# Kernel optimization log

Measured on AMD Instinct MI355X. Metric: run time of the kernel, lower is better.

The kernel has to match this reference:

```python
import jax, jax.numpy as jnp
import numpy as np

N_NODES = 100000


def _gcn_conv(x, W, b, src, dst, n):
    # PyG GCNConv: add self-loops, sym-normalize by deg^{-1/2}, then X W + b
    h = x @ W  # [N, out]
    ones = jnp.ones(src.shape[0], dtype=x.dtype)
    deg = jax.ops.segment_sum(ones, dst, num_segments=n) + 1.0  # +1 for self loop
    dinv = jax.lax.rsqrt(deg)
    norm = dinv[src] * dinv[dst]  # [E]
    agg = jax.ops.segment_sum(h[src] * norm[:, None], dst, num_segments=n)
    agg = agg + h * (dinv * dinv)[:, None]  # self-loop contribution
    return agg + b


def setup_inputs() -> dict:
    key = jax.random.key(0)
    k1, k2, k3, k4 = jax.random.split(key, 4)
    n, e = N_NODES, 1600000
    in_d, hid_d, out_d = 128, 128, 64
    x = jax.random.normal(k1, (n, in_d), dtype=jnp.float32)
    edge_index = jax.random.randint(k2, (2, e), 0, n, dtype=jnp.int64)
    s1 = 1.0 / np.sqrt(in_d)
    s2 = 1.0 / np.sqrt(hid_d)
    W1 = jax.random.uniform(k3, (in_d, hid_d), jnp.float32, -s1, s1)
    W2 = jax.random.uniform(k4, (hid_d, out_d), jnp.float32, -s2, s2)
    b1 = jnp.zeros((hid_d,), jnp.float32)
    b2 = jnp.zeros((out_d,), jnp.float32)
    return {"x": x, "edge_index": edge_index, "W1": W1, "b1": b1, "W2": W2, "b2": b2}


def reference(x, edge_index, W1, b1, W2, b2):
    src, dst = edge_index[0], edge_index[1]
    n = x.shape[0]
    h = _gcn_conv(x, W1, b1, src, dst, n)
    h = jax.nn.relu(h)
    # dropout p=0.2 is identity at eval time
    out = _gcn_conv(h, W2, b2, src, dst, n)
    return out
```

## Files before the change

### kernel.cpp

```cpp
#include <hip/hip_runtime.h>


typedef unsigned int u32;
using bfrag = __attribute__((ext_vector_type(8))) short;
using f4    = __attribute__((ext_vector_type(4))) float;

__device__ inline u32 pack_bf16(float a, float b) {
    u32 ua = __float_as_uint(a);
    u32 ub = __float_as_uint(b);
    ua += 0x7fffu + ((ua >> 16) & 1u);
    ub += 0x7fffu + ((ub >> 16) & 1u);
    return (ua >> 16) | (ub & 0xffff0000u);
}
__device__ inline float bf_lo(u32 v) { return __uint_as_float(v << 16); }
__device__ inline float bf_hi(u32 v) { return __uint_as_float(v & 0xffff0000u); }

__device__ inline u32 pack_w(float w) {
    u32 b = __float_as_uint(w) + 0x800u;
    if (b < 0x3B800000u) b = 0x3B800000u;
    if (b > 0x3F800000u) b = 0x3F800000u;
    return (b - 0x3B800000u) >> 12;
}
__device__ inline float dec_w(u32 e) {
    return __uint_as_float(((e & 0x7fffu) << 12) + 0x3B800000u);
}

__device__ inline bfrag as_bfrag(uint4 v) {
    union { uint4 u; bfrag b; } x; x.u = v; return x.b;
}


__global__ __launch_bounds__(256) void count_bins(const int* __restrict__ dst,
                                                  int* __restrict__ bc,
                                                  int E, int nbin, int nb3) {
    __shared__ int hist[512];
    for (int t = threadIdx.x; t < nbin; t += 256) hist[t] = 0;
    __syncthreads();
    const int base = blockIdx.x * 2048 + threadIdx.x;
#pragma unroll
    for (int k = 0; k < 8; ++k) {
        int e = base + k * 256;
        if (e < E) atomicAdd(&hist[dst[e] >> 8], 1);
    }
    __syncthreads();
    for (int t = threadIdx.x; t < nbin; t += 256)
        bc[(size_t)t * nb3 + blockIdx.x] = hist[t];
}

__global__ __launch_bounds__(1024) void scan_reduce_g(const int* __restrict__ a,
                                                      int* __restrict__ bsum, int M) {
    __shared__ int wsum[16];
    int i = blockIdx.x * 1024 + threadIdx.x;
    int v = (i < M) ? a[i] : 0;
#pragma unroll
    for (int off = 32; off > 0; off >>= 1) v += __shfl_down(v, off);
    const int lane = threadIdx.x & 63;
    const int wid  = threadIdx.x >> 6;
    if (lane == 0) wsum[wid] = v;
    __syncthreads();
    if (threadIdx.x < 16) {
        int s = wsum[threadIdx.x];
#pragma unroll
        for (int off = 8; off > 0; off >>= 1) s += __shfl_down(s, off);
        if (threadIdx.x == 0) bsum[blockIdx.x] = s;
    }
}

__global__ void scan_partials(const int* __restrict__ bsum, int* __restrict__ boff,
                              int* __restrict__ total_out, int nb) {
    const int lane = threadIdx.x;
    int carry = 0;
    for (int base = 0; base < nb; base += 64) {
        int i = base + lane;
        int v = (i < nb) ? bsum[i] : 0;
        int x = v;
#pragma unroll
        for (int off = 1; off < 64; off <<= 1) {
            int t = __shfl_up(x, off);
            if (lane >= off) x += t;
        }
        if (i < nb) boff[i] = carry + x - v;
        carry += __shfl(x, 63);
    }
    if (lane == 0) *total_out = carry;
}

__global__ __launch_bounds__(1024) void scan_apply_g(int* __restrict__ a,
                                                     const int* __restrict__ boff, int M) {
    __shared__ int wsum[16];
    const int lane = threadIdx.x & 63;
    const int wid  = threadIdx.x >> 6;
    int i = blockIdx.x * 1024 + threadIdx.x;
    int v = (i < M) ? a[i] : 0;
    int x = v;
#pragma unroll
    for (int off = 1; off < 64; off <<= 1) {
        int t = __shfl_up(x, off);
        if (lane >= off) x += t;
    }
    if (lane == 63) wsum[wid] = x;
    __syncthreads();
    if (wid == 0 && lane < 16) {
        int w = wsum[lane];
#pragma unroll
        for (int off = 1; off < 16; off <<= 1) {
            int t = __shfl_up(w, off);
            if (lane >= off) w += t;
        }
        wsum[lane] = w;
    }
    __syncthreads();
    int wave_excl = (wid == 0) ? 0 : wsum[wid - 1];
    if (i < M) a[i] = boff[blockIdx.x] + wave_excl + (x - v);
}

__global__ __launch_bounds__(1024) void scan_apply_cnt(const int* __restrict__ cnt,
                                                       const int* __restrict__ boff,
                                                       int* __restrict__ row_ptr,
                                                       float* __restrict__ dinv, int n) {
    __shared__ int wsum[16];
    const int lane = threadIdx.x & 63;
    const int wid  = threadIdx.x >> 6;
    int i = blockIdx.x * 1024 + threadIdx.x;
    int v = (i < n) ? cnt[i] : 0;
    int x = v;
#pragma unroll
    for (int off = 1; off < 64; off <<= 1) {
        int t = __shfl_up(x, off);
        if (lane >= off) x += t;
    }
    if (lane == 63) wsum[wid] = x;
    __syncthreads();
    if (wid == 0 && lane < 16) {
        int w = wsum[lane];
#pragma unroll
        for (int off = 1; off < 16; off <<= 1) {
            int t = __shfl_up(w, off);
            if (lane >= off) w += t;
        }
        wsum[lane] = w;
    }
    __syncthreads();
    int wave_excl = (wid == 0) ? 0 : wsum[wid - 1];
    if (i < n) {
        row_ptr[i] = boff[blockIdx.x] + wave_excl + (x - v);
        dinv[i]    = rsqrtf((float)v + 1.0f);
    }
}

__global__ __launch_bounds__(256) void scatter_bins(const int* __restrict__ src,
                                                    const int* __restrict__ dst,
                                                    const int* __restrict__ offs,
                                                    u32* __restrict__ tmp,
                                                    int E, int nbin, int nb3) {
    __shared__ int cur[512];
    for (int t = threadIdx.x; t < nbin; t += 256)
        cur[t] = offs[(size_t)t * nb3 + blockIdx.x];
    __syncthreads();
    const int base = blockIdx.x * 2048 + threadIdx.x;
#pragma unroll
    for (int k = 0; k < 8; ++k) {
        int e = base + k * 256;
        if (e < E) {
            int d = dst[e];
            int pos = atomicAdd(&cur[d >> 8], 1);
            tmp[pos] = ((u32)(d & 255) << 17) | (u32)src[e];
        }
    }
}

__global__ __launch_bounds__(256) void bucket_csr(const u32* __restrict__ tmp,
                                                  const int* __restrict__ offs,
                                                  u32* __restrict__ tmp3,
                                                  int* __restrict__ cnt,
                                                  int n, int nb3) {
    __shared__ int hist[256];
    __shared__ int cur[256];
    __shared__ int wtot[4];
    const int b   = blockIdx.x;
    const int beg = offs[(size_t)b * nb3];
    const int end = offs[(size_t)(b + 1) * nb3];
    hist[threadIdx.x] = 0;
    __syncthreads();
    for (int i = beg + threadIdx.x; i < end; i += 256)
        atomicAdd(&hist[tmp[i] >> 17], 1);
    __syncthreads();
    const int lane = threadIdx.x & 63;
    const int wid  = threadIdx.x >> 6;
    int v = hist[threadIdx.x];
    int x = v;
#pragma unroll
    for (int off = 1; off < 64; off <<= 1) {
        int t = __shfl_up(x, off);
        if (lane >= off) x += t;
    }
    if (lane == 63) wtot[wid] = x;
    __syncthreads();
    int wbase = 0;
    for (int w = 0; w < wid; ++w) wbase += wtot[w];
    cur[threadIdx.x] = beg + wbase + x - v;
    int d = b * 256 + threadIdx.x;
    if (d < n) cnt[d] = v;
    __syncthreads();
    for (int i = beg + threadIdx.x; i < end; i += 256) {
        u32 r = tmp[i];
        int pos = atomicAdd(&cur[r >> 17], 1);
        tmp3[pos] = r & 0x1ffffu;
    }
}

__global__ __launch_bounds__(256) void build_ew(const u32* __restrict__ tmp3,
                                                const int* __restrict__ row_ptr,
                                                const float* __restrict__ dinv,
                                                u32* __restrict__ ew, int n) {
    int d = blockIdx.x * 256 + threadIdx.x;
    if (d >= n) return;
    float dd = dinv[d];
    int beg = row_ptr[d], end = row_ptr[d + 1];
    for (int i = beg; i < end; ++i) {
        u32 s = tmp3[i];
        ew[i] = (s << 15) | pack_w(dinv[s] * dd);
    }
}


__global__ void prep_w(const float* __restrict__ W1, const float* __restrict__ W2,
                       u32* __restrict__ W1t, u32* __restrict__ W2t) {
    int idx = blockIdx.x * 256 + threadIdx.x;
    if (idx < 128 * 64) {
        int nr = idx >> 6, kd = idx & 63;
        W1t[idx] = pack_bf16(W1[(2 * kd) * 128 + nr], W1[(2 * kd + 1) * 128 + nr]);
    } else if (idx < 128 * 64 + 64 * 64) {
        int i = idx - 128 * 64;
        int nr = i >> 6, kd = i & 63;
        W2t[i] = pack_bf16(W2[(2 * kd) * 64 + nr], W2[(2 * kd + 1) * 64 + nr]);
    }
}

template <int OUT, bool ABF>
__global__ __launch_bounds__(256) void gemm_mfma(const void* __restrict__ Ap,
                                                 const u32* __restrict__ Wt,
                                                 u32* __restrict__ C, int n) {
    constexpr int NT = OUT / 16;
    const int lane = threadIdx.x & 63;
    const int wv   = threadIdx.x >> 6;
    const int r15  = lane & 15;
    const int quad = lane >> 4;
    const int rowbase = blockIdx.x * 128 + wv * 32;

    bfrag af[2][4];
#pragma unroll
    for (int mi = 0; mi < 2; ++mi) {
        int row = rowbase + mi * 16 + r15;
        row = (row < n) ? row : (n - 1);
        if constexpr (ABF) {
            const u32* ar = (const u32*)Ap + (size_t)row * 64 + quad * 4;
#pragma unroll
            for (int ks = 0; ks < 4; ++ks)
                af[mi][ks] = as_bfrag(*(const uint4*)(ar + ks * 16));
        } else {
            const float* arf = (const float*)Ap + (size_t)row * 128 + quad * 8;
#pragma unroll
            for (int ks = 0; ks < 4; ++ks) {
                float4 v0 = *(const float4*)(arf + ks * 32);
                float4 v1 = *(const float4*)(arf + ks * 32 + 4);
                uint4 p;
                p.x = pack_bf16(v0.x, v0.y);
                p.y = pack_bf16(v0.z, v0.w);
                p.z = pack_bf16(v1.x, v1.y);
                p.w = pack_bf16(v1.z, v1.w);
                af[mi][ks] = as_bfrag(p);
            }
        }
    }

    f4 acc[2][NT];
#pragma unroll
    for (int mi = 0; mi < 2; ++mi)
#pragma unroll
        for (int nt = 0; nt < NT; ++nt) acc[mi][nt] = (f4)0.0f;

#pragma unroll
    for (int nt = 0; nt < NT; ++nt) {
        const u32* wr = Wt + (size_t)(nt * 16 + r15) * 64 + quad * 4;
#pragma unroll
        for (int ks = 0; ks < 4; ++ks) {
            bfrag bf = as_bfrag(*(const uint4*)(wr + ks * 16));
            acc[0][nt] = __builtin_amdgcn_mfma_f32_16x16x32_bf16(bf, af[0][ks], acc[0][nt], 0, 0, 0);
            acc[1][nt] = __builtin_amdgcn_mfma_f32_16x16x32_bf16(bf, af[1][ks], acc[1][nt], 0, 0, 0);
        }
    }

#pragma unroll
    for (int mi = 0; mi < 2; ++mi) {
        int row = rowbase + mi * 16 + r15;
        if (row < n) {
            u32* cp = C + (size_t)row * (OUT / 2);
#pragma unroll
            for (int nt = 0; nt < NT; ++nt) {
                uint2 p;
                p.x = pack_bf16(acc[mi][nt][0], acc[mi][nt][1]);
                p.y = pack_bf16(acc[mi][nt][2], acc[mi][nt][3]);
                *(uint2*)(cp + nt * 8 + quad * 2) = p;
            }
        }
    }
}


__global__ __launch_bounds__(256) void gather128(const u32* __restrict__ h,
                                                 const float* __restrict__ dinv,
                                                 const int* __restrict__ row_ptr,
                                                 const u32* __restrict__ ew,
                                                 const float* __restrict__ bias,
                                                 u32* __restrict__ outp, int n) {
    const int lane = threadIdx.x & 63;
    int node = blockIdx.x * 4 + (threadIdx.x >> 6);
    if (node >= n) return;
    node = __builtin_amdgcn_readfirstlane(node);

    const float dd  = dinv[node];
    const int   beg = __builtin_amdgcn_readfirstlane(row_ptr[node]);
    const int   end = __builtin_amdgcn_readfirstlane(row_ptr[node + 1]);

    u32 sv = h[(size_t)node * 64 + lane];
    float2 b = ((const float2*)bias)[lane];
    float acc0 = fmaf(bf_lo(sv) * dd, dd, b.x);
    float acc1 = fmaf(bf_hi(sv) * dd, dd, b.y);

    int j = beg;
    for (; j + 16 <= end; j += 16) {
        u32 ep[16];
#pragma unroll
        for (int k = 0; k < 16; ++k) ep[k] = ew[j + k];
        u32 v[16];
#pragma unroll
        for (int k = 0; k < 16; ++k)
            v[k] = h[((size_t)(ep[k] >> 15) << 6) + lane];
#pragma unroll
        for (int k = 0; k < 16; ++k) {
            float wf = dec_w(ep[k]);
            acc0 = fmaf(wf, bf_lo(v[k]), acc0);
            acc1 = fmaf(wf, bf_hi(v[k]), acc1);
        }
    }
    for (; j < end; j += 8) {
        const int cnt = end - j;
        u32 ep[8];
#pragma unroll
        for (int k = 0; k < 8; ++k) {
            int c = j + k;
            ep[k] = ew[(c < end) ? c : end - 1];
        }
        u32 v[8];
#pragma unroll
        for (int k = 0; k < 8; ++k)
            v[k] = h[((size_t)(ep[k] >> 15) << 6) + lane];
#pragma unroll
        for (int k = 0; k < 8; ++k) {
            float wf = (k < cnt) ? dec_w(ep[k]) : 0.0f;
            acc0 = fmaf(wf, bf_lo(v[k]), acc0);
            acc1 = fmaf(wf, bf_hi(v[k]), acc1);
        }
    }

    outp[(size_t)node * 64 + lane] = pack_bf16(fmaxf(acc0, 0.0f), fmaxf(acc1, 0.0f));
}

__global__ __launch_bounds__(256) void gather64(const u32* __restrict__ h,
                                                const float* __restrict__ dinv,
                                                const int* __restrict__ row_ptr,
                                                const u32* __restrict__ ew,
                                                const float* __restrict__ bias,
                                                float* __restrict__ outp, int n) {
    const int lane   = threadIdx.x & 63;
    const int lane32 = lane & 31;
    const int sub    = lane >> 5;
    int node = blockIdx.x * 4 + (threadIdx.x >> 6);
    if (node >= n) return;
    node = __builtin_amdgcn_readfirstlane(node);

    const int beg = __builtin_amdgcn_readfirstlane(row_ptr[node]);
    const int end = __builtin_amdgcn_readfirstlane(row_ptr[node + 1]);

    float acc0 = 0.0f, acc1 = 0.0f;
    if (sub == 0) {
        const float dd = dinv[node];
        u32 sv = h[(size_t)node * 32 + lane32];
        float2 b = ((const float2*)bias)[lane32];
        acc0 = fmaf(bf_lo(sv) * dd, dd, b.x);
        acc1 = fmaf(bf_hi(sv) * dd, dd, b.y);
    }

    int j = beg;
    for (; j + 8 <= end; j += 8) {
        u32 ep[8];
#pragma unroll
        for (int k = 0; k < 8; ++k) ep[k] = ew[j + k];
        u32 v[4]; float wl[4];
#pragma unroll
        for (int p = 0; p < 4; ++p) {
            u32 e0 = ep[2 * p], e1 = ep[2 * p + 1];
            u32 so = sub ? (e1 >> 15) : (e0 >> 15);
            wl[p]  = sub ? dec_w(e1) : dec_w(e0);
            v[p]   = h[((size_t)so << 5) + lane32];
        }
#pragma unroll
        for (int p = 0; p < 4; ++p) {
            acc0 = fmaf(wl[p], bf_lo(v[p]), acc0);
            acc1 = fmaf(wl[p], bf_hi(v[p]), acc1);
        }
    }
    for (; j < end; j += 8) {
        const int cnt = end - j;
        u32 ep[8];
#pragma unroll
        for (int k = 0; k < 8; ++k) {
            int c = j + k;
            ep[k] = ew[(c < end) ? c : end - 1];
        }
        u32 v[4]; float wl[4];
#pragma unroll
        for (int p = 0; p < 4; ++p) {
            u32 e0 = ep[2 * p], e1 = ep[2 * p + 1];
            float w0 = (2 * p     < cnt) ? dec_w(e0) : 0.0f;
            float w1 = (2 * p + 1 < cnt) ? dec_w(e1) : 0.0f;
            u32 so = sub ? (e1 >> 15) : (e0 >> 15);
            wl[p]  = sub ? w1 : w0;
            v[p]   = h[((size_t)so << 5) + lane32];
        }
#pragma unroll
        for (int p = 0; p < 4; ++p) {
            acc0 = fmaf(wl[p], bf_lo(v[p]), acc0);
            acc1 = fmaf(wl[p], bf_hi(v[p]), acc1);
        }
    }

    acc0 += __shfl_xor(acc0, 32);
    acc1 += __shfl_xor(acc1, 32);
    if (sub == 0)
        ((float2*)(outp + (size_t)node * 64))[lane32] = make_float2(acc0, acc1);
}

extern "C" void kernel_launch(void* const* d_in, const int* in_sizes, int n_in,
                              void* d_out, int out_size, void* d_ws, size_t ws_size,
                              hipStream_t stream) {
    const float* x  = (const float*)d_in[0];
    const int*   ei = (const int*)d_in[1];
    const float* W1 = (const float*)d_in[2];
    const float* b1 = (const float*)d_in[3];
    const float* W2 = (const float*)d_in[4];
    const float* b2 = (const float*)d_in[5];
    float*       out = (float*)d_out;

    const int n = in_sizes[0] / 128;
    const int E = in_sizes[1] / 2;
    const int* srcv = ei;
    const int* dstv = ei + E;

    const int NP = 102400;
    u32* wsd = (u32*)d_ws;
    float* dinv    = (float*)wsd;
    int*   row_ptr = (int*)(wsd + NP);
    u32*   ew      = wsd + 2 * (size_t)NP;
    u32*   h1u     = ew + E;
    u32*   agg1b   = h1u + (size_t)n * 64;
    u32*   W1t     = agg1b + (size_t)n * 64;
    u32*   W2t     = W1t + 8192;
    u32*   h2u     = h1u;

    int*   cnt  = (int*)h1u;
    int*   bco  = (int*)(h1u + 131072);
    u32*   tmp2 = h1u + 524288;
    u32*   tmp3 = tmp2 + (size_t)E;
    int*   bsum = (int*)(h1u + 4000000);
    int*   boff = bsum + 512;

    const int NBIN = (n + 255) >> 8;
    const int NB3  = (E + 2047) / 2048;
    const int M    = NBIN * NB3;
    const int MB   = (M + 1023) / 1024;
    const int NB   = (n + 1023) / 1024;

    count_bins<<<NB3, 256, 0, stream>>>(dstv, bco, E, NBIN, NB3);
    scan_reduce_g<<<MB, 1024, 0, stream>>>(bco, bsum, M);
    scan_partials<<<1, 64, 0, stream>>>(bsum, boff, bco + M, MB);
    scan_apply_g<<<MB, 1024, 0, stream>>>(bco, boff, M);
    scatter_bins<<<NB3, 256, 0, stream>>>(srcv, dstv, bco, tmp2, E, NBIN, NB3);
    bucket_csr<<<NBIN, 256, 0, stream>>>(tmp2, bco, tmp3, cnt, n, NB3);
    scan_reduce_g<<<NB, 1024, 0, stream>>>(cnt, bsum, n);
    scan_partials<<<1, 64, 0, stream>>>(bsum, boff, row_ptr + n, NB);
    scan_apply_cnt<<<NB, 1024, 0, stream>>>(cnt, boff, row_ptr, dinv, n);
    build_ew<<<(n + 255) / 256, 256, 0, stream>>>(tmp3, row_ptr, dinv, ew, n);

    prep_w<<<48, 256, 0, stream>>>(W1, W2, W1t, W2t);

    const int gblocks = (n + 127) / 128;
    gemm_mfma<128, false><<<gblocks, 256, 0, stream>>>(x, W1t, h1u, n);
    gather128<<<(n + 3) / 4, 256, 0, stream>>>(h1u, dinv, row_ptr, ew, b1, agg1b, n);

    gemm_mfma<64, true><<<gblocks, 256, 0, stream>>>(agg1b, W2t, h2u, n);
    gather64<<<(n + 3) / 4, 256, 0, stream>>>(h2u, dinv, row_ptr, ew, b2, out, n);
}
```

Baseline: 313.2 us.

## Slice feature matrices into 16-column slabs for cache-local gathers

The GEMMs now write their bf16 outputs in a slab layout: each 16-feature slice of all nodes is stored contiguously (32 bytes per node). The gathers are rewritten so each block handles one slice, with 8 lanes per edge covering 8 edges at once, and reduce across lanes with shuffles. This keeps each slab (about 3.2 MB) small enough to stay cache-resident during the random neighbour reads. In exchange, the edge list and row pointers are re-read once per slice, and each random access fetches only 32 bytes.

```diff
diff --git a/kernel.cpp b/kernel.cpp
--- a/kernel.cpp
+++ b/kernel.cpp
@@ -24,6 +24,8 @@
 __device__ inline float dec_w(u32 e) {
     return __uint_as_float(((e & 0x7fffu) << 12) + 0x3B800000u);
 }
+
+__device__ inline int rfl(int v) { return __builtin_amdgcn_readfirstlane(v); }
 
 __device__ inline bfrag as_bfrag(uint4 v) {
     union { uint4 u; bfrag b; } x; x.u = v; return x.b;
@@ -240,7 +242,8 @@
 template <int OUT, bool ABF>
 __global__ __launch_bounds__(256) void gemm_mfma(const void* __restrict__ Ap,
                                                  const u32* __restrict__ Wt,
-                                                 u32* __restrict__ C, int n) {
+                                                 u32* __restrict__ C, int n,
+                                                 size_t aslab, size_t cslab) {
     constexpr int NT = OUT / 16;
     const int lane = threadIdx.x & 63;
     const int wv   = threadIdx.x >> 6;
@@ -254,10 +257,10 @@
         int row = rowbase + mi * 16 + r15;
         row = (row < n) ? row : (n - 1);
         if constexpr (ABF) {
-            const u32* ar = (const u32*)Ap + (size_t)row * 64 + quad * 4;
+            const u32* ar = (const u32*)Ap + (size_t)row * 8 + (quad & 1) * 4;
 #pragma unroll
             for (int ks = 0; ks < 4; ++ks)
-                af[mi][ks] = as_bfrag(*(const uint4*)(ar + ks * 16));
+                af[mi][ks] = as_bfrag(*(const uint4*)(ar + (size_t)(ks * 2 + (quad >> 1)) * aslab));
         } else {
             const float* arf = (const float*)Ap + (size_t)row * 128 + quad * 8;
 #pragma unroll
@@ -295,151 +298,116 @@
     for (int mi = 0; mi < 2; ++mi) {
         int row = rowbase + mi * 16 + r15;
         if (row < n) {
-            u32* cp = C + (size_t)row * (OUT / 2);
+            u32* cp = C + (size_t)row * 8 + quad * 2;
 #pragma unroll
             for (int nt = 0; nt < NT; ++nt) {
                 uint2 p;
                 p.x = pack_bf16(acc[mi][nt][0], acc[mi][nt][1]);
                 p.y = pack_bf16(acc[mi][nt][2], acc[mi][nt][3]);
-                *(uint2*)(cp + nt * 8 + quad * 2) = p;
+                *(uint2*)(cp + (size_t)nt * cslab) = p;
             }
         }
     }
 }
 
 
-__global__ __launch_bounds__(256) void gather128(const u32* __restrict__ h,
+__global__ __launch_bounds__(256) void gather128s(const u32* __restrict__ h,
+                                                  const float* __restrict__ dinv,
+                                                  const int* __restrict__ row_ptr,
+                                                  const u32* __restrict__ ew,
+                                                  const float* __restrict__ bias,
+                                                  u32* __restrict__ outp, int n) {
+    const int lane  = threadIdx.x & 63;
+    const int wid   = rfl(threadIdx.x >> 6);
+    const int slice = blockIdx.x & 7;
+    const int grp   = blockIdx.x >> 3;
+    const int es = lane >> 3, dw = lane & 7;
+    const size_t SLAB = (size_t)n * 8;
+    const u32* hs = h + (size_t)slice * SLAB;
+    u32* os = outp + (size_t)slice * SLAB;
+    const float2 b = ((const float2*)bias)[slice * 8 + dw];
+
+    const int node0 = (grp * 4 + wid) * 4;
+#pragma unroll 1
+    for (int ni = 0; ni < 4; ++ni) {
+        const int node = node0 + ni;
+        if (node >= n) return;
+        const int beg = rfl(row_ptr[node]);
+        const int end = rfl(row_ptr[node + 1]);
+        float acc0 = 0.0f, acc1 = 0.0f;
+        for (int j0 = beg; j0 < end; j0 += 16) {
+            int jA = j0 + es,     cA = (jA < end) ? jA : end - 1;
+            int jB = j0 + 8 + es, cB = (jB < end) ? jB : end - 1;
+            u32 eA = __builtin_nontemporal_load(ew + cA);
+            u32 eB = __builtin_nontemporal_load(ew + cB);
+            u32 vA = hs[(size_t)(eA >> 15) * 8 + dw];
+            u32 vB = hs[(size_t)(eB >> 15) * 8 + dw];
+            float wA = (jA < end) ? dec_w(eA) : 0.0f;
+            float wB = (jB < end) ? dec_w(eB) : 0.0f;
+            acc0 = fmaf(wA, bf_lo(vA), acc0); acc1 = fmaf(wA, bf_hi(vA), acc1);
+            acc0 = fmaf(wB, bf_lo(vB), acc0); acc1 = fmaf(wB, bf_hi(vB), acc1);
+        }
+        acc0 += __shfl_xor(acc0, 8);  acc1 += __shfl_xor(acc1, 8);
+        acc0 += __shfl_xor(acc0, 16); acc1 += __shfl_xor(acc1, 16);
+        acc0 += __shfl_xor(acc0, 32); acc1 += __shfl_xor(acc1, 32);
+        if (es == 0) {
+            const float dd = dinv[node];
+            u32 sv = hs[(size_t)node * 8 + dw];
+            acc0 += fmaf(bf_lo(sv) * dd, dd, b.x);
+            acc1 += fmaf(bf_hi(sv) * dd, dd, b.y);
+            os[(size_t)node * 8 + dw] = pack_bf16(fmaxf(acc0, 0.0f), fmaxf(acc1, 0.0f));
+        }
+    }
+}
+
+__global__ __launch_bounds__(256) void gather64s(const u32* __restrict__ h,
                                                  const float* __restrict__ dinv,
                                                  const int* __restrict__ row_ptr,
                                                  const u32* __restrict__ ew,
                                                  const float* __restrict__ bias,
-                                                 u32* __restrict__ outp, int n) {
-    const int lane = threadIdx.x & 63;
-    int node = blockIdx.x * 4 + (threadIdx.x >> 6);
-    if (node >= n) return;
-    node = __builtin_amdgcn_readfirstlane(node);
-
-    const float dd  = dinv[node];
-    const int   beg = __builtin_amdgcn_readfirstlane(row_ptr[node]);
-    const int   end = __builtin_amdgcn_readfirstlane(row_ptr[node + 1]);
-
-    u32 sv = h[(size_t)node * 64 + lane];
-    float2 b = ((const float2*)bias)[lane];
-    float acc0 = fmaf(bf_lo(sv) * dd, dd, b.x);
-    float acc1 = fmaf(bf_hi(sv) * dd, dd, b.y);
-
-    int j = beg;
-    for (; j + 16 <= end; j += 16) {
-        u32 ep[16];
-#pragma unroll
-        for (int k = 0; k < 16; ++k) ep[k] = ew[j + k];
-        u32 v[16];
-#pragma unroll
-        for (int k = 0; k < 16; ++k)
-            v[k] = h[((size_t)(ep[k] >> 15) << 6) + lane];
-#pragma unroll
-        for (int k = 0; k < 16; ++k) {
-            float wf = dec_w(ep[k]);
-            acc0 = fmaf(wf, bf_lo(v[k]), acc0);
-            acc1 = fmaf(wf, bf_hi(v[k]), acc1);
-        }
-    }
-    for (; j < end; j += 8) {
-        const int cnt = end - j;
-        u32 ep[8];
-#pragma unroll
-        for (int k = 0; k < 8; ++k) {
-            int c = j + k;
-            ep[k] = ew[(c < end) ? c : end - 1];
-        }
-        u32 v[8];
-#pragma unroll
-        for (int k = 0; k < 8; ++k)
-            v[k] = h[((size_t)(ep[k] >> 15) << 6) + lane];
-#pragma unroll
-        for (int k = 0; k < 8; ++k) {
-            float wf = (k < cnt) ? dec_w(ep[k]) : 0.0f;
-            acc0 = fmaf(wf, bf_lo(v[k]), acc0);
-            acc1 = fmaf(wf, bf_hi(v[k]), acc1);
-        }
-    }
-
-    outp[(size_t)node * 64 + lane] = pack_bf16(fmaxf(acc0, 0.0f), fmaxf(acc1, 0.0f));
-}
-
-__global__ __launch_bounds__(256) void gather64(const u32* __restrict__ h,
-                                                const float* __restrict__ dinv,
-                                                const int* __restrict__ row_ptr,
-                                                const u32* __restrict__ ew,
-                                                const float* __restrict__ bias,
-                                                float* __restrict__ outp, int n) {
-    const int lane   = threadIdx.x & 63;
-    const int lane32 = lane & 31;
-    const int sub    = lane >> 5;
-    int node = blockIdx.x * 4 + (threadIdx.x >> 6);
-    if (node >= n) return;
-    node = __builtin_amdgcn_readfirstlane(node);
-
-    const int beg = __builtin_amdgcn_readfirstlane(row_ptr[node]);
-    const int end = __builtin_amdgcn_readfirstlane(row_ptr[node + 1]);
-
-    float acc0 = 0.0f, acc1 = 0.0f;
-    if (sub == 0) {
-        const float dd = dinv[node];
-        u32 sv = h[(size_t)node * 32 + lane32];
-        float2 b = ((const float2*)bias)[lane32];
-        acc0 = fmaf(bf_lo(sv) * dd, dd, b.x);
-        acc1 = fmaf(bf_hi(sv) * dd, dd, b.y);
-    }
-
-    int j = beg;
-    for (; j + 8 <= end; j += 8) {
-        u32 ep[8];
-#pragma unroll
-        for (int k = 0; k < 8; ++k) ep[k] = ew[j + k];
-        u32 v[4]; float wl[4];
-#pragma unroll
-        for (int p = 0; p < 4; ++p) {
-            u32 e0 = ep[2 * p], e1 = ep[2 * p + 1];
-            u32 so = sub ? (e1 >> 15) : (e0 >> 15);
-            wl[p]  = sub ? dec_w(e1) : dec_w(e0);
-            v[p]   = h[((size_t)so << 5) + lane32];
-        }
-#pragma unroll
-        for (int p = 0; p < 4; ++p) {
-            acc0 = fmaf(wl[p], bf_lo(v[p]), acc0);
-            acc1 = fmaf(wl[p], bf_hi(v[p]), acc1);
-        }
-    }
-    for (; j < end; j += 8) {
-        const int cnt = end - j;
-        u32 ep[8];
-#pragma unroll
-        for (int k = 0; k < 8; ++k) {
-            int c = j + k;
-            ep[k] = ew[(c < end) ? c : end - 1];
-        }
-        u32 v[4]; float wl[4];
-#pragma unroll
-        for (int p = 0; p < 4; ++p) {
-            u32 e0 = ep[2 * p], e1 = ep[2 * p + 1];
-            float w0 = (2 * p     < cnt) ? dec_w(e0) : 0.0f;
-            float w1 = (2 * p + 1 < cnt) ? dec_w(e1) : 0.0f;
-            u32 so = sub ? (e1 >> 15) : (e0 >> 15);
-            wl[p]  = sub ? w1 : w0;
-            v[p]   = h[((size_t)so << 5) + lane32];
-        }
-#pragma unroll
-        for (int p = 0; p < 4; ++p) {
-            acc0 = fmaf(wl[p], bf_lo(v[p]), acc0);
-            acc1 = fmaf(wl[p], bf_hi(v[p]), acc1);
-        }
-    }
-
-    acc0 += __shfl_xor(acc0, 32);
-    acc1 += __shfl_xor(acc1, 32);
-    if (sub == 0)
-        ((float2*)(outp + (size_t)node * 64))[lane32] = make_float2(acc0, acc1);
+                                                 float* __restrict__ outp, int n) {
+    const int lane  = threadIdx.x & 63;
+    const int wid   = rfl(threadIdx.x >> 6);
+    const int x8    = blockIdx.x & 7;
+    const int slice = x8 & 3;
+    const int half  = x8 >> 2;
+    const int grp   = blockIdx.x >> 3;
+    const int es = lane >> 3, dw = lane & 7;
+    const size_t SLAB = (size_t)n * 8;
+    const u32* hs = h + (size_t)slice * SLAB;
+    const float2 b = ((const float2*)bias)[slice * 8 + dw];
+
+    const int node0 = ((grp * 2 + half) * 4 + wid) * 4;
+#pragma unroll 1
+    for (int ni = 0; ni < 4; ++ni) {
+        const int node = node0 + ni;
+        if (node >= n) return;
+        const int beg = rfl(row_ptr[node]);
+        const int end = rfl(row_ptr[node + 1]);
+        float acc0 = 0.0f, acc1 = 0.0f;
+        for (int j0 = beg; j0 < end; j0 += 16) {
+            int jA = j0 + es,     cA = (jA < end) ? jA : end - 1;
+            int jB = j0 + 8 + es, cB = (jB < end) ? jB : end - 1;
+            u32 eA = __builtin_nontemporal_load(ew + cA);
+            u32 eB = __builtin_nontemporal_load(ew + cB);
+            u32 vA = hs[(size_t)(eA >> 15) * 8 + dw];
+            u32 vB = hs[(size_t)(eB >> 15) * 8 + dw];
+            float wA = (jA < end) ? dec_w(eA) : 0.0f;
+            float wB = (jB < end) ? dec_w(eB) : 0.0f;
+            acc0 = fmaf(wA, bf_lo(vA), acc0); acc1 = fmaf(wA, bf_hi(vA), acc1);
+            acc0 = fmaf(wB, bf_lo(vB), acc0); acc1 = fmaf(wB, bf_hi(vB), acc1);
+        }
+        acc0 += __shfl_xor(acc0, 8);  acc1 += __shfl_xor(acc1, 8);
+        acc0 += __shfl_xor(acc0, 16); acc1 += __shfl_xor(acc1, 16);
+        acc0 += __shfl_xor(acc0, 32); acc1 += __shfl_xor(acc1, 32);
+        if (es == 0) {
+            const float dd = dinv[node];
+            u32 sv = hs[(size_t)node * 8 + dw];
+            acc0 += fmaf(bf_lo(sv) * dd, dd, b.x);
+            acc1 += fmaf(bf_hi(sv) * dd, dd, b.y);
+            ((float2*)(outp + (size_t)node * 64 + slice * 16))[dw] = make_float2(acc0, acc1);
+        }
+    }
 }
 
 extern "C" void kernel_launch(void* const* d_in, const int* in_sizes, int n_in,
@@ -495,10 +463,11 @@
 
     prep_w<<<48, 256, 0, stream>>>(W1, W2, W1t, W2t);
 
+    const size_t SLAB = (size_t)n * 8;
     const int gblocks = (n + 127) / 128;
-    gemm_mfma<128, false><<<gblocks, 256, 0, stream>>>(x, W1t, h1u, n);
-    gather128<<<(n + 3) / 4, 256, 0, stream>>>(h1u, dinv, row_ptr, ew, b1, agg1b, n);
-
-    gemm_mfma<64, true><<<gblocks, 256, 0, stream>>>(agg1b, W2t, h2u, n);
-    gather64<<<(n + 3) / 4, 256, 0, stream>>>(h2u, dinv, row_ptr, ew, b2, out, n);
-}
+    gemm_mfma<128, false><<<gblocks, 256, 0, stream>>>(x, W1t, h1u, n, 0, SLAB);
+    gather128s<<<((n + 15) / 16) * 8, 256, 0, stream>>>(h1u, dinv, row_ptr, ew, b1, agg1b, n);
+
+    gemm_mfma<64, true><<<gblocks, 256, 0, stream>>>(agg1b, W2t, h2u, n, SLAB, SLAB);
+    gather64s<<<((n + 31) / 32) * 8, 256, 0, stream>>>(h2u, dinv, row_ptr, ew, b2, out, n);
+}
```

Result: slower. 522.9 us (+67.0%).

## Cut scan launches, fold weight prep into count kernel, unroll gather by 16

Applied to the files above, without the earlier changes.

Merges the weight bf16 packing into the bin-counting kernel as extra blocks, removing a separate launch. The single-wave partial-scan kernel is dropped: each scan block now sums the preceding block totals itself. The node-count scan reuses bin offsets already computed (each 1024-node block starts at bin 4*blockIdx, offset at column 0), which removes three launches. The first gather loop's unroll goes from 8 to 16 edges for more loads in flight, at the cost of more registers and a longer tail for low-degree nodes.

```diff
diff --git a/kernel.cpp b/kernel.cpp
--- a/kernel.cpp
+++ b/kernel.cpp
@@ -30,10 +30,27 @@
 }
 
 
-__global__ __launch_bounds__(256) void count_bins(const int* __restrict__ dst,
-                                                  int* __restrict__ bc,
-                                                  int E, int nbin, int nb3) {
+__global__ __launch_bounds__(256) void count_bins_pw(const int* __restrict__ dst,
+                                                     int* __restrict__ bc,
+                                                     int E, int nbin, int nb3, int M,
+                                                     const float* __restrict__ W1,
+                                                     const float* __restrict__ W2,
+                                                     u32* __restrict__ W1t,
+                                                     u32* __restrict__ W2t) {
     __shared__ int hist[512];
+    if (blockIdx.x >= (unsigned)nb3) {
+        int idx = (blockIdx.x - nb3) * 256 + threadIdx.x;
+        if (idx < 128 * 64) {
+            int nr = idx >> 6, kd = idx & 63;
+            W1t[idx] = pack_bf16(W1[(2 * kd) * 128 + nr], W1[(2 * kd + 1) * 128 + nr]);
+        } else if (idx < 128 * 64 + 64 * 64) {
+            int i = idx - 128 * 64;
+            int nr = i >> 6, kd = i & 63;
+            W2t[i] = pack_bf16(W2[(2 * kd) * 64 + nr], W2[(2 * kd + 1) * 64 + nr]);
+        }
+        return;
+    }
+    if (blockIdx.x == 0 && threadIdx.x == 0) bc[M] = E;
     for (int t = threadIdx.x; t < nbin; t += 256) hist[t] = 0;
     __syncthreads();
     const int base = blockIdx.x * 2048 + threadIdx.x;
@@ -66,32 +83,64 @@
     }
 }
 
-__global__ void scan_partials(const int* __restrict__ bsum, int* __restrict__ boff,
-                              int* __restrict__ total_out, int nb) {
-    const int lane = threadIdx.x;
-    int carry = 0;
-    for (int base = 0; base < nb; base += 64) {
-        int i = base + lane;
-        int v = (i < nb) ? bsum[i] : 0;
-        int x = v;
-#pragma unroll
-        for (int off = 1; off < 64; off <<= 1) {
-            int t = __shfl_up(x, off);
-            if (lane >= off) x += t;
-        }
-        if (i < nb) boff[i] = carry + x - v;
-        carry += __shfl(x, 63);
-    }
-    if (lane == 0) *total_out = carry;
-}
-
-__global__ __launch_bounds__(1024) void scan_apply_g(int* __restrict__ a,
-                                                     const int* __restrict__ boff, int M) {
+__global__ __launch_bounds__(1024) void scan_apply_g2(int* __restrict__ a,
+                                                      const int* __restrict__ bsum,
+                                                      int nb, int M) {
+    __shared__ int wsum[16];
+    __shared__ int base_s;
+    const int lane = threadIdx.x & 63;
+    const int wid  = threadIdx.x >> 6;
+
+    int pv = 0;
+    for (int t = threadIdx.x; t < (int)blockIdx.x; t += 1024) pv += bsum[t];
+#pragma unroll
+    for (int off = 32; off > 0; off >>= 1) pv += __shfl_down(pv, off);
+    if (lane == 0) wsum[wid] = pv;
+    __syncthreads();
+    if (threadIdx.x == 0) {
+        int s = 0;
+#pragma unroll
+        for (int w = 0; w < 16; ++w) s += wsum[w];
+        base_s = s;
+    }
+    __syncthreads();
+    const int boff = base_s;
+
+    int i = blockIdx.x * 1024 + threadIdx.x;
+    int v = (i < M) ? a[i] : 0;
+    int x = v;
+#pragma unroll
+    for (int off = 1; off < 64; off <<= 1) {
+        int t = __shfl_up(x, off);
+        if (lane >= off) x += t;
+    }
+    if (lane == 63) wsum[wid] = x;
+    __syncthreads();
+    if (wid == 0 && lane < 16) {
+        int w = wsum[lane];
+#pragma unroll
+        for (int off = 1; off < 16; off <<= 1) {
+            int t = __shfl_up(w, off);
+            if (lane >= off) w += t;
+        }
+        wsum[lane] = w;
+    }
+    __syncthreads();
+    int wave_excl = (wid == 0) ? 0 : wsum[wid - 1];
+    if (i < M) a[i] = boff + wave_excl + (x - v);
+}
+
+__global__ __launch_bounds__(1024) void scan_apply_cnt2(const int* __restrict__ cnt,
+                                                        const int* __restrict__ bco,
+                                                        int* __restrict__ row_ptr,
+                                                        float* __restrict__ dinv,
+                                                        int n, int nb3, int E) {
     __shared__ int wsum[16];
     const int lane = threadIdx.x & 63;
     const int wid  = threadIdx.x >> 6;
+    const int boff = bco[(size_t)(4 * blockIdx.x) * nb3];
     int i = blockIdx.x * 1024 + threadIdx.x;
-    int v = (i < M) ? a[i] : 0;
+    int v = (i < n) ? cnt[i] : 0;
     int x = v;
 #pragma unroll
     for (int off = 1; off < 64; off <<= 1) {
@@ -111,41 +160,11 @@
     }
     __syncthreads();
     int wave_excl = (wid == 0) ? 0 : wsum[wid - 1];
-    if (i < M) a[i] = boff[blockIdx.x] + wave_excl + (x - v);
-}
-
-__global__ __launch_bounds__(1024) void scan_apply_cnt(const int* __restrict__ cnt,
-                                                       const int* __restrict__ boff,
-                                                       int* __restrict__ row_ptr,
-                                                       float* __restrict__ dinv, int n) {
-    __shared__ int wsum[16];
-    const int lane = threadIdx.x & 63;
-    const int wid  = threadIdx.x >> 6;
-    int i = blockIdx.x * 1024 + threadIdx.x;
-    int v = (i < n) ? cnt[i] : 0;
-    int x = v;
-#pragma unroll
-    for (int off = 1; off < 64; off <<= 1) {
-        int t = __shfl_up(x, off);
-        if (lane >= off) x += t;
-    }
-    if (lane == 63) wsum[wid] = x;
-    __syncthreads();
-    if (wid == 0 && lane < 16) {
-        int w = wsum[lane];
-#pragma unroll
-        for (int off = 1; off < 16; off <<= 1) {
-            int t = __shfl_up(w, off);
-            if (lane >= off) w += t;
-        }
-        wsum[lane] = w;
-    }
-    __syncthreads();
-    int wave_excl = (wid == 0) ? 0 : wsum[wid - 1];
     if (i < n) {
-        row_ptr[i] = boff[blockIdx.x] + wave_excl + (x - v);
+        row_ptr[i] = boff + wave_excl + (x - v);
         dinv[i]    = rsqrtf((float)v + 1.0f);
     }
+    if (blockIdx.x == 0 && threadIdx.x == 0) row_ptr[n] = E;
 }
 
 __global__ __launch_bounds__(256) void scatter_bins(const int* __restrict__ src,
@@ -224,19 +243,6 @@
 }
 
 
-__global__ void prep_w(const float* __restrict__ W1, const float* __restrict__ W2,
-                       u32* __restrict__ W1t, u32* __restrict__ W2t) {
-    int idx = blockIdx.x * 256 + threadIdx.x;
-    if (idx < 128 * 64) {
-        int nr = idx >> 6, kd = idx & 63;
-        W1t[idx] = pack_bf16(W1[(2 * kd) * 128 + nr], W1[(2 * kd + 1) * 128 + nr]);
-    } else if (idx < 128 * 64 + 64 * 64) {
-        int i = idx - 128 * 64;
-        int nr = i >> 6, kd = i & 63;
-        W2t[i] = pack_bf16(W2[(2 * kd) * 64 + nr], W2[(2 * kd + 1) * 64 + nr]);
-    }
-}
-
 template <int OUT, bool ABF>
 __global__ __launch_bounds__(256) void gemm_mfma(const void* __restrict__ Ap,
                                                  const u32* __restrict__ Wt,
@@ -393,20 +399,20 @@
     }
 
     int j = beg;
-    for (; j + 8 <= end; j += 8) {
-        u32 ep[8];
-#pragma unroll
-        for (int k = 0; k < 8; ++k) ep[k] = ew[j + k];
-        u32 v[4]; float wl[4];
-#pragma unroll
-        for (int p = 0; p < 4; ++p) {
+    for (; j + 16 <= end; j += 16) {
+        u32 ep[16];
+#pragma unroll
+        for (int k = 0; k < 16; ++k) ep[k] = ew[j + k];
+        u32 v[8]; float wl[8];
+#pragma unroll
+        for (int p = 0; p < 8; ++p) {
             u32 e0 = ep[2 * p], e1 = ep[2 * p + 1];
             u32 so = sub ? (e1 >> 15) : (e0 >> 15);
             wl[p]  = sub ? dec_w(e1) : dec_w(e0);
             v[p]   = h[((size_t)so << 5) + lane32];
         }
 #pragma unroll
-        for (int p = 0; p < 4; ++p) {
+        for (int p = 0; p < 8; ++p) {
             acc0 = fmaf(wl[p], bf_lo(v[p]), acc0);
             acc1 = fmaf(wl[p], bf_hi(v[p]), acc1);
         }
@@ -474,7 +480,6 @@
     u32*   tmp2 = h1u + 524288;
     u32*   tmp3 = tmp2 + (size_t)E;
     int*   bsum = (int*)(h1u + 4000000);
-    int*   boff = bsum + 512;
 
     const int NBIN = (n + 255) >> 8;
     const int NB3  = (E + 2047) / 2048;
@@ -482,18 +487,14 @@
     const int MB   = (M + 1023) / 1024;
     const int NB   = (n + 1023) / 1024;
 
-    count_bins<<<NB3, 256, 0, stream>>>(dstv, bco, E, NBIN, NB3);
+    count_bins_pw<<<NB3 + 48, 256, 0, stream>>>(dstv, bco, E, NBIN, NB3, M,
+                                                W1, W2, W1t, W2t);
     scan_reduce_g<<<MB, 1024, 0, stream>>>(bco, bsum, M);
-    scan_partials<<<1, 64, 0, stream>>>(bsum, boff, bco + M, MB);
-    scan_apply_g<<<MB, 1024, 0, stream>>>(bco, boff, M);
+    scan_apply_g2<<<MB, 1024, 0, stream>>>(bco, bsum, MB, M);
     scatter_bins<<<NB3, 256, 0, stream>>>(srcv, dstv, bco, tmp2, E, NBIN, NB3);
     bucket_csr<<<NBIN, 256, 0, stream>>>(tmp2, bco, tmp3, cnt, n, NB3);
-    scan_reduce_g<<<NB, 1024, 0, stream>>>(cnt, bsum, n);
-    scan_partials<<<1, 64, 0, stream>>>(bsum, boff, row_ptr + n, NB);
-    scan_apply_cnt<<<NB, 1024, 0, stream>>>(cnt, boff, row_ptr, dinv, n);
+    scan_apply_cnt2<<<NB, 1024, 0, stream>>>(cnt, bco, row_ptr, dinv, n, NB3, E);
     build_ew<<<(n + 255) / 256, 256, 0, stream>>>(tmp3, row_ptr, dinv, ew, n);
-
-    prep_w<<<48, 256, 0, stream>>>(W1, W2, W1t, W2t);
 
     const int gblocks = (n + 127) / 128;
     gemm_mfma<128, false><<<gblocks, 256, 0, stream>>>(x, W1t, h1u, n);
```

New measurement: 302.0 us. 1.04x faster.
